# Optimization experiments

Hardware: AMD Instinct MI355X
Metric: run time of the kernel (lower is better)

The kernel has to match this reference:

```python
import jax, jax.numpy as jnp
import numpy as np

N = 500_000  # n_nodes == n_edges (required by the broadcast out * norm[:, None])
C_IN = 128
C_OUT = 128


def setup_inputs() -> dict:
    key = jax.random.key(0)
    k_x, k_e, k_w, k_b = jax.random.split(key, 4)
    x = jax.random.normal(k_x, (N, C_IN), dtype=jnp.float32)
    edge_index = jax.random.randint(k_e, (2, N), 0, N, dtype=jnp.int64)
    # Linear(in_channels, out_channels): weight [out, in], bias [out]
    bound = 1.0 / np.sqrt(C_IN)
    W = jax.random.uniform(k_w, (C_OUT, C_IN), minval=-bound, maxval=bound, dtype=jnp.float32)
    b = jax.random.uniform(k_b, (C_OUT,), minval=-bound, maxval=bound, dtype=jnp.float32)
    return {"x": x, "edge_index": edge_index, "W": W, "b": b}


def reference(x, edge_index, W, b):
    row, col = edge_index[0], edge_index[1]  # each [E], with E == N
    n = x.shape[0]
    out = x @ W.T + b  # [N, C_OUT]
    # degree via scatter-add of ones over row
    deg = jax.ops.segment_sum(jnp.ones(row.shape[0], dtype=x.dtype), row, num_segments=n)
    deg_inv_sqrt = jnp.where(deg > 0, jax.lax.rsqrt(jnp.where(deg > 0, deg, 1.0)), 0.0)
    norm = deg_inv_sqrt[row] * deg_inv_sqrt[col]  # [E] == [N]
    out = out * norm[:, None]  # broadcast relies on E == N (as in the torch source)
    # aggregated[row] += out[col]
    aggregated = jnp.zeros_like(out).at[row].add(out[col])
    return aggregated
```

## Files before the change

kernel.cpp:

```cpp
#include <hip/hip_runtime.h>

#define C 128

typedef __bf16 bf16_t;
typedef bf16_t bf16x8 __attribute__((ext_vector_type(8)));
typedef float f32x4 __attribute__((ext_vector_type(4)));

__global__ void deg_kernel(const int* __restrict__ row, int* __restrict__ deg, int e) {
    int i = blockIdx.x * blockDim.x + threadIdx.x;
    if (i < e) atomicAdd(&deg[row[i]], 1);
}

__global__ void wcvt_kernel(const float* __restrict__ W, bf16_t* __restrict__ Wb) {
    int i = blockIdx.x * blockDim.x + threadIdx.x;
    if (i < C * C) Wb[i] = (bf16_t)W[i];
}

__global__ __launch_bounds__(256) void scan1_kernel(const int* __restrict__ deg,
                                                    float* __restrict__ dis,
                                                    int* __restrict__ offs,
                                                    int* __restrict__ partials, int n) {
    __shared__ int s[256];
    const int tid = threadIdx.x;
    const int base = blockIdx.x * 1024 + tid * 4;
    int v[4];
    #pragma unroll
    for (int j = 0; j < 4; ++j) v[j] = (base + j < n) ? deg[base + j] : 0;
    #pragma unroll
    for (int j = 0; j < 4; ++j)
        if (base + j < n) dis[base + j] = v[j] > 0 ? rsqrtf((float)v[j]) : 0.f;
    int tsum = v[0] + v[1] + v[2] + v[3];
    s[tid] = tsum;
    __syncthreads();
    for (int off = 1; off < 256; off <<= 1) {
        int t = (tid >= off) ? s[tid - off] : 0;
        __syncthreads();
        s[tid] += t;
        __syncthreads();
    }
    int excl = s[tid] - tsum;
    #pragma unroll
    for (int j = 0; j < 4; ++j) {
        if (base + j < n) offs[base + j] = excl;
        excl += v[j];
    }
    if (tid == 255) partials[blockIdx.x] = s[255];
}

__global__ __launch_bounds__(1024) void scan2_kernel(int* __restrict__ partials, int nb) {
    __shared__ int s[1024];
    const int tid = threadIdx.x;
    int v = (tid < nb) ? partials[tid] : 0;
    s[tid] = v;
    __syncthreads();
    for (int off = 1; off < 1024; off <<= 1) {
        int t = (tid >= off) ? s[tid - off] : 0;
        __syncthreads();
        s[tid] += t;
        __syncthreads();
    }
    if (tid < nb) partials[tid] = s[tid] - v;
}

__global__ void norm_kernel(const int* __restrict__ row, const int* __restrict__ col,
                            const float* __restrict__ dis, float* __restrict__ nrm, int e) {
    int i = blockIdx.x * blockDim.x + threadIdx.x;
    if (i < e) nrm[i] = dis[row[i]] * dis[col[i]];
}

__global__ void bucket_kernel(const int* __restrict__ row, const int* __restrict__ col,
                              const int* __restrict__ offs, const int* __restrict__ partials,
                              const float* __restrict__ nrm, int* __restrict__ cursor,
                              int2* __restrict__ csr_cw, int e) {
    int i = blockIdx.x * blockDim.x + threadIdx.x;
    if (i < e) {
        int r = row[i];
        int c = col[i];
        int pos = atomicAdd(&cursor[r], 1);
        int idx = offs[r] + partials[r >> 10] + pos;
        csr_cw[idx] = make_int2(c, __float_as_int(nrm[c]));
    }
}

__global__ __launch_bounds__(256, 4) void fused_kernel(
        const f32x4* __restrict__ x4, const int2* __restrict__ csr_cw,
        const int* __restrict__ offs, const int* __restrict__ partials,
        const int* __restrict__ deg, const bf16x8* __restrict__ Wb8,
        const float* __restrict__ bias, float* __restrict__ out, int n)
{
    const int lane = threadIdx.x & 63;
    const int wave = threadIdx.x >> 6;
    const int m    = lane & 15;
    const int quad = lane >> 4;
    const long r0  = ((long)blockIdx.x * 4 + wave) * 16;
    if (r0 >= n) return;
    const int  r  = (int)r0 + m;
    const bool rv = r < n;
    const int  d     = rv ? deg[r] : 0;
    const int  start = rv ? offs[r] + partials[r >> 10] : 0;

    f32x4 acc[8];
    #pragma unroll
    for (int i = 0; i < 8; ++i) acc[i] = (f32x4){0.f, 0.f, 0.f, 0.f};
    float sw = 0.f;

    int k = 0;
    for (; k + 2 <= d; k += 2) {
        const int2 cw0 = csr_cw[start + k];
        const int2 cw1 = csr_cw[start + k + 1];
        const float w0 = __int_as_float(cw0.y);
        const float w1 = __int_as_float(cw1.y);
        sw += w0 + w1;
        const f32x4* xr0 = x4 + (long)cw0.x * 32 + quad * 2;
        const f32x4* xr1 = x4 + (long)cw1.x * 32 + quad * 2;
        #pragma unroll
        for (int kc = 0; kc < 4; ++kc) {
            f32x4 u0 = xr0[kc * 8];
            f32x4 u1 = xr0[kc * 8 + 1];
            f32x4 v0 = xr1[kc * 8];
            f32x4 v1 = xr1[kc * 8 + 1];
            acc[kc * 2]     += w0 * u0;
            acc[kc * 2 + 1] += w0 * u1;
            acc[kc * 2]     += w1 * v0;
            acc[kc * 2 + 1] += w1 * v1;
        }
    }
    if (k < d) {
        const int2 cw = csr_cw[start + k];
        const float w = __int_as_float(cw.y);
        sw += w;
        const f32x4* xr = x4 + (long)cw.x * 32 + quad * 2;
        #pragma unroll
        for (int kc = 0; kc < 4; ++kc) {
            f32x4 u0 = xr[kc * 8];
            f32x4 u1 = xr[kc * 8 + 1];
            acc[kc * 2]     += w * u0;
            acc[kc * 2 + 1] += w * u1;
        }
    }

    bf16x8 a[4];
    #pragma unroll
    for (int kc = 0; kc < 4; ++kc) {
        #pragma unroll
        for (int j = 0; j < 4; ++j) {
            a[kc][j]     = (bf16_t)acc[kc * 2][j];
            a[kc][j + 4] = (bf16_t)acc[kc * 2 + 1][j];
        }
    }

    float cv[4];
    #pragma unroll
    for (int v = 0; v < 4; ++v) cv[v] = __shfl(sw, quad * 4 + v);

    for (int t = 0; t < 8; ++t) {
        const int o = t * 16 + m;
        bf16x8 bf[4];
        #pragma unroll
        for (int kc = 0; kc < 4; ++kc)
            bf[kc] = Wb8[(long)o * 16 + kc * 4 + quad];
        f32x4 cacc = {0.f, 0.f, 0.f, 0.f};
        #pragma unroll
        for (int kc = 0; kc < 4; ++kc)
            cacc = __builtin_amdgcn_mfma_f32_16x16x32_bf16(a[kc], bf[kc], cacc, 0, 0, 0);
        const float bb = bias[o];
        #pragma unroll
        for (int v = 0; v < 4; ++v) {
            const long rr = r0 + quad * 4 + v;
            if (rr < n)
                __builtin_nontemporal_store(cacc[v] + cv[v] * bb, &out[rr * C + o]);
        }
    }
}

extern "C" void kernel_launch(void* const* d_in, const int* in_sizes, int n_in,
                              void* d_out, int out_size, void* d_ws, size_t ws_size,
                              hipStream_t stream) {
    const float* x  = (const float*)d_in[0];
    const int*   ei = (const int*)d_in[1];
    const float* W  = (const float*)d_in[2];
    const float* b  = (const float*)d_in[3];
    float* out = (float*)d_out;

    const int n = in_sizes[0] / C;
    const int e = in_sizes[1] / 2;
    const int* row = ei;
    const int* col = ei + e;

    int*   deg_i    = (int*)d_ws;
    int*   cursor   = deg_i + n;
    int*   offs     = cursor + n;
    int2*  csr_cw   = (int2*)(offs + n);
    float* dis      = (float*)(csr_cw + e);
    float* nrm      = dis + n;
    int*   partials = (int*)(nrm + e);
    bf16_t* Wb      = (bf16_t*)dis;

    const int nb = (n + 1023) / 1024;

    hipMemsetAsync(deg_i, 0, (size_t)2 * n * sizeof(int), stream);

    deg_kernel<<<(e + 255) / 256, 256, 0, stream>>>(row, deg_i, e);
    scan1_kernel<<<nb, 256, 0, stream>>>(deg_i, dis, offs, partials, n);
    scan2_kernel<<<1, 1024, 0, stream>>>(partials, nb);
    norm_kernel<<<(e + 255) / 256, 256, 0, stream>>>(row, col, dis, nrm, e);
    wcvt_kernel<<<(C * C + 255) / 256, 256, 0, stream>>>(W, Wb);
    bucket_kernel<<<(e + 255) / 256, 256, 0, stream>>>(row, col, offs, partials, nrm,
                                                       cursor, csr_cw, e);

    int blocks = (n + 63) / 64;
    fused_kernel<<<blocks, 256, 0, stream>>>(
        (const f32x4*)x, csr_cw, offs, partials, deg_i,
        (const bf16x8*)Wb, b, out, n);
}
```

Before: 608.3 us.

## Sort rows by degree bins for balanced waves; compute edge norm inside bucketing

Adds a 32-bin degree histogram to the scan pass and a new permute kernel that counting-sorts node indices by degree. The fused aggregate-plus-GEMM kernel then processes rows in this permuted order, so the 16 rows in a wave have similar degree and the gather loop diverges less. It writes output rows back through the permutation. The separate norm kernel and its array are removed: the weight is now computed inline in the bucket kernel from dis, with workspace reused for the histogram, the permutation and the bf16 weights. The trade-off is an extra kernel and scattered output-row stores instead of contiguous 16-row blocks.

```diff
diff --git a/kernel.cpp b/kernel.cpp
--- a/kernel.cpp
+++ b/kernel.cpp
@@ -19,9 +19,12 @@
 __global__ __launch_bounds__(256) void scan1_kernel(const int* __restrict__ deg,
                                                     float* __restrict__ dis,
                                                     int* __restrict__ offs,
-                                                    int* __restrict__ partials, int n) {
+                                                    int* __restrict__ partials,
+                                                    int* __restrict__ dhist, int n) {
     __shared__ int s[256];
+    __shared__ int dh[32];
     const int tid = threadIdx.x;
+    if (tid < 32) dh[tid] = 0;
     const int base = blockIdx.x * 1024 + tid * 4;
     int v[4];
     #pragma unroll
@@ -32,6 +35,9 @@
     int tsum = v[0] + v[1] + v[2] + v[3];
     s[tid] = tsum;
     __syncthreads();
+    #pragma unroll
+    for (int j = 0; j < 4; ++j)
+        if (base + j < n) atomicAdd(&dh[min(v[j], 31)], 1);
     for (int off = 1; off < 256; off <<= 1) {
         int t = (tid >= off) ? s[tid - off] : 0;
         __syncthreads();
@@ -45,9 +51,12 @@
         excl += v[j];
     }
     if (tid == 255) partials[blockIdx.x] = s[255];
-}
-
-__global__ __launch_bounds__(1024) void scan2_kernel(int* __restrict__ partials, int nb) {
+    if (tid < 32 && dh[tid] > 0) atomicAdd(&dhist[tid], dh[tid]);
+}
+
+__global__ __launch_bounds__(1024) void scan2_kernel(int* __restrict__ partials,
+                                                     const int* __restrict__ dhist,
+                                                     int* __restrict__ drun, int nb) {
     __shared__ int s[1024];
     const int tid = threadIdx.x;
     int v = (tid < nb) ? partials[tid] : 0;
@@ -60,33 +69,60 @@
         __syncthreads();
     }
     if (tid < nb) partials[tid] = s[tid] - v;
-}
-
-__global__ void norm_kernel(const int* __restrict__ row, const int* __restrict__ col,
-                            const float* __restrict__ dis, float* __restrict__ nrm, int e) {
-    int i = blockIdx.x * blockDim.x + threadIdx.x;
-    if (i < e) nrm[i] = dis[row[i]] * dis[col[i]];
+    if (tid < 64) {
+        int h = (tid < 32) ? dhist[tid] : 0;
+        int c = h;
+        #pragma unroll
+        for (int off = 1; off < 32; off <<= 1) {
+            int t = __shfl_up(c, off);
+            if (tid >= off) c += t;
+        }
+        if (tid < 32) drun[tid] = c - h;
+    }
+}
+
+__global__ __launch_bounds__(256) void permute_kernel(const int* __restrict__ deg,
+                                                      int* __restrict__ drun,
+                                                      int* __restrict__ perm, int n) {
+    __shared__ int lh[32], lb[32];
+    const int tid = threadIdx.x;
+    const int i = blockIdx.x * 256 + tid;
+    if (tid < 32) lh[tid] = 0;
+    __syncthreads();
+    int bin = 0, lr = 0;
+    const bool valid = i < n;
+    if (valid) {
+        int d = deg[i];
+        bin = min(d, 31);
+        lr = atomicAdd(&lh[bin], 1);
+    }
+    __syncthreads();
+    if (tid < 32 && lh[tid] > 0) lb[tid] = atomicAdd(&drun[tid], lh[tid]);
+    __syncthreads();
+    if (valid) perm[lb[bin] + lr] = i;
 }
 
 __global__ void bucket_kernel(const int* __restrict__ row, const int* __restrict__ col,
                               const int* __restrict__ offs, const int* __restrict__ partials,
-                              const float* __restrict__ nrm, int* __restrict__ cursor,
+                              const float* __restrict__ dis, int* __restrict__ cursor,
                               int2* __restrict__ csr_cw, int e) {
     int i = blockIdx.x * blockDim.x + threadIdx.x;
     if (i < e) {
         int r = row[i];
         int c = col[i];
+        float w = dis[row[c]] * dis[col[c]];
         int pos = atomicAdd(&cursor[r], 1);
         int idx = offs[r] + partials[r >> 10] + pos;
-        csr_cw[idx] = make_int2(c, __float_as_int(nrm[c]));
+        csr_cw[idx] = make_int2(c, __float_as_int(w));
     }
 }
 
 __global__ __launch_bounds__(256, 4) void fused_kernel(
         const f32x4* __restrict__ x4, const int2* __restrict__ csr_cw,
         const int* __restrict__ offs, const int* __restrict__ partials,
-        const int* __restrict__ deg, const bf16x8* __restrict__ Wb8,
-        const float* __restrict__ bias, float* __restrict__ out, int n)
+        const int* __restrict__ deg, const int* __restrict__ perm,
+        const bf16x8* __restrict__ Wb8, const float* __restrict__ bias,
+        float* __restrict__ out, int n)
 {
     const int lane = threadIdx.x & 63;
     const int wave = threadIdx.x >> 6;
@@ -94,10 +130,11 @@
     const int quad = lane >> 4;
     const long r0  = ((long)blockIdx.x * 4 + wave) * 16;
     if (r0 >= n) return;
-    const int  r  = (int)r0 + m;
-    const bool rv = r < n;
-    const int  d     = rv ? deg[r] : 0;
-    const int  start = rv ? offs[r] + partials[r >> 10] : 0;
+    const int  pi = (int)r0 + m;
+    const bool rv = pi < n;
+    const int  prow  = rv ? perm[pi] : 0;
+    const int  d     = rv ? deg[prow] : 0;
+    const int  start = rv ? offs[prow] + partials[prow >> 10] : 0;
 
     f32x4 acc[8];
     #pragma unroll
@@ -150,8 +187,12 @@
     }
 
     float cv[4];
-    #pragma unroll
-    for (int v = 0; v < 4; ++v) cv[v] = __shfl(sw, quad * 4 + v);
+    int   orow[4];
+    #pragma unroll
+    for (int v = 0; v < 4; ++v) {
+        cv[v]   = __shfl(sw, quad * 4 + v);
+        orow[v] = __shfl(prow, quad * 4 + v);
+    }
 
     for (int t = 0; t < 8; ++t) {
         const int o = t * 16 + m;
@@ -166,9 +207,9 @@
         const float bb = bias[o];
         #pragma unroll
         for (int v = 0; v < 4; ++v) {
-            const long rr = r0 + quad * 4 + v;
-            if (rr < n)
-                __builtin_nontemporal_store(cacc[v] + cv[v] * bb, &out[rr * C + o]);
+            if (r0 + quad * 4 + v < n)
+                __builtin_nontemporal_store(cacc[v] + cv[v] * bb,
+                                            &out[(long)orow[v] * C + o]);
         }
     }
 }
@@ -192,24 +233,27 @@
     int*   offs     = cursor + n;
     int2*  csr_cw   = (int2*)(offs + n);
     float* dis      = (float*)(csr_cw + e);
-    float* nrm      = dis + n;
-    int*   partials = (int*)(nrm + e);
-    bf16_t* Wb      = (bf16_t*)dis;
+    int*   perm     = (int*)(dis + n);
+    int*   partials = perm + n;
+    int*   dhist    = (int*)csr_cw;
+    int*   drun     = dhist + 32;
+    bf16_t* Wb      = (bf16_t*)cursor;
 
     const int nb = (n + 1023) / 1024;
 
     hipMemsetAsync(deg_i, 0, (size_t)2 * n * sizeof(int), stream);
+    hipMemsetAsync(dhist, 0, 64 * sizeof(int), stream);
 
     deg_kernel<<<(e + 255) / 256, 256, 0, stream>>>(row, deg_i, e);
-    scan1_kernel<<<nb, 256, 0, stream>>>(deg_i, dis, offs, partials, n);
-    scan2_kernel<<<1, 1024, 0, stream>>>(partials, nb);
-    norm_kernel<<<(e + 255) / 256, 256, 0, stream>>>(row, col, dis, nrm, e);
+    scan1_kernel<<<nb, 256, 0, stream>>>(deg_i, dis, offs, partials, dhist, n);
+    scan2_kernel<<<1, 1024, 0, stream>>>(partials, dhist, drun, nb);
+    permute_kernel<<<(n + 255) / 256, 256, 0, stream>>>(deg_i, drun, perm, n);
+    bucket_kernel<<<(e + 255) / 256, 256, 0, stream>>>(row, col, offs, partials, dis,
+                                                       cursor, csr_cw, e);
     wcvt_kernel<<<(C * C + 255) / 256, 256, 0, stream>>>(W, Wb);
-    bucket_kernel<<<(e + 255) / 256, 256, 0, stream>>>(row, col, offs, partials, nrm,
-                                                       cursor, csr_cw, e);
 
     int blocks = (n + 63) / 64;
     fused_kernel<<<blocks, 256, 0, stream>>>(
-        (const f32x4*)x, csr_cw, offs, partials, deg_i,
+        (const f32x4*)x, csr_cw, offs, partials, deg_i, perm,
         (const bf16x8*)Wb, b, out, n);
 }
```

Result: slower. 622.2 us (+2.3%).
